# Optimization experiments

Measured on AMD Instinct MI355X. Metric: run time of the kernel, lower is better.

The kernel has to match this reference:

```python
import jax, jax.numpy as jnp
import numpy as np


def chamfer_bidirectional(p1, p2):
    """p1: [B,N,3], p2: [B,M,3]. Returns (min_sq_dist1 [B,N], min_sq_dist2 [B,M])."""
    # squared pairwise distances via ||a||^2 + ||b||^2 - 2 a.b  (avoids [B,N,M,3] diff tensor)
    n1 = jnp.sum(p1 * p1, axis=-1)          # [B,N]
    n2 = jnp.sum(p2 * p2, axis=-1)          # [B,M]
    cross = jnp.einsum('bnd,bmd->bnm', p1, p2)  # [B,N,M]
    d = n1[:, :, None] + n2[:, None, :] - 2.0 * cross  # [B,N,M]
    d = jnp.maximum(d, 0.0)
    return jnp.min(d, axis=2), jnp.min(d, axis=1)


def setup_inputs() -> dict:
    key = jax.random.key(0)
    k1, k2, k3, k4, k5 = jax.random.split(key, 5)
    B = 8
    return {
        'pred': jax.random.normal(k1, (B, 10, 3), dtype=jnp.float32),
        'target': jax.random.normal(k2, (B, 10, 3), dtype=jnp.float32),
        'coarse': jax.random.normal(k3, (B, 3, 1024), dtype=jnp.float32),
        'fine': jax.random.normal(k4, (B, 3, 4096), dtype=jnp.float32),
        'gt_pc': jax.random.normal(k5, (B, 4096, 3), dtype=jnp.float32),
    }


def reference(pred, target, coarse, fine, gt_pc):
    kp_loss = jnp.mean((pred - target) ** 2)
    c1, c2 = chamfer_bidirectional(jnp.transpose(coarse, (0, 2, 1)), gt_pc)
    f1, f2 = chamfer_bidirectional(jnp.transpose(fine, (0, 2, 1)), gt_pc)
    coarse_loss = jnp.mean(c1) + jnp.mean(c2)
    fine_loss = jnp.mean(f1) + jnp.mean(f2)
    return kp_loss + coarse_loss + fine_loss
```

## Files before the change

kernel.cpp:

```cpp
#include <hip/hip_runtime.h>
#include <math.h>

#define SBMAX 2112

template<int CHUNK, bool A_PLANAR, bool B_PLANAR>
__device__ __forceinline__ float chamfer_block(
    const float* __restrict__ A, int An,
    const float* __restrict__ B, int Bn,
    int lbid, float scale,
    float (&sb)[4][SBMAX], float (&red)[512])
{
    constexpr int NSEG    = 16;
    constexpr int SEG     = CHUNK / NSEG;
    constexpr int LOG_SEG = (CHUNK == 2048) ? 7 : 6;
    constexpr int SEGP    = SEG + 4;

    const int bpb   = An >> 5;
    const int batch = lbid / bpb;
    const int ablk  = lbid % bpb;
    const float* __restrict__ Ab = A + (size_t)batch * 3 * An;
    const float* __restrict__ Bb = B + (size_t)batch * 3 * Bn;

    const int tid  = threadIdx.x;
    const int slot = tid & 15;
    const int sp   = tid >> 4;
    const int p0   = ablk * 32 + slot;
    const int p1   = p0 + 16;

    float a0x, a0y, a0z, a1x, a1y, a1z;
    if (A_PLANAR) {
        a0x = Ab[p0];   a0y = Ab[An + p0];  a0z = Ab[2*An + p0];
        a1x = Ab[p1];   a1y = Ab[An + p1];  a1z = Ab[2*An + p1];
    } else {
        a0x = Ab[3*p0]; a0y = Ab[3*p0 + 1]; a0z = Ab[3*p0 + 2];
        a1x = Ab[3*p1]; a1y = Ab[3*p1 + 1]; a1z = Ab[3*p1 + 2];
    }
    const float a0s = fmaf(a0x, a0x, fmaf(a0y, a0y, a0z * a0z));
    const float a1s = fmaf(a1x, a1x, fmaf(a1y, a1y, a1z * a1z));

    const float BIG = 3.402823466e38f;
    float n00 = BIG, n01 = BIG, n10 = BIG, n11 = BIG;

    for (int t0 = 0; t0 < Bn; t0 += CHUNK) {
#pragma unroll
        for (int i = 0; i < CHUNK / 256; ++i) {
            const int k = tid + i * 256;
            float x, y, z;
            if (B_PLANAR) {
                x = Bb[t0 + k]; y = Bb[Bn + t0 + k]; z = Bb[2*Bn + t0 + k];
            } else {
                int base = 3 * (t0 + k);
                x = Bb[base]; y = Bb[base + 1]; z = Bb[base + 2];
            }
            const int addr = (k >> LOG_SEG) * SEGP + (k & (SEG - 1));
            sb[0][addr] = -2.0f * x;
            sb[1][addr] = -2.0f * y;
            sb[2][addr] = -2.0f * z;
            sb[3][addr] = fmaf(x, x, fmaf(y, y, z * z));
        }
        __syncthreads();

        const float4* __restrict__ px = (const float4*)&sb[0][sp * SEGP];
        const float4* __restrict__ py = (const float4*)&sb[1][sp * SEGP];
        const float4* __restrict__ pz = (const float4*)&sb[2][sp * SEGP];
        const float4* __restrict__ pw = (const float4*)&sb[3][sp * SEGP];
#pragma unroll 2
        for (int g = 0; g < SEG / 4; ++g) {
            float4 x = px[g], y = py[g], z = pz[g], w = pw[g];
            float d0, d1, d2, d3;
            d0 = fmaf(a0x, x.x, fmaf(a0y, y.x, fmaf(a0z, z.x, w.x)));
            d1 = fmaf(a0x, x.y, fmaf(a0y, y.y, fmaf(a0z, z.y, w.y)));
            d2 = fmaf(a0x, x.z, fmaf(a0y, y.z, fmaf(a0z, z.z, w.z)));
            d3 = fmaf(a0x, x.w, fmaf(a0y, y.w, fmaf(a0z, z.w, w.w)));
            n00 = fminf(fminf(d0, d1), n00);
            n01 = fminf(fminf(d2, d3), n01);
            d0 = fmaf(a1x, x.x, fmaf(a1y, y.x, fmaf(a1z, z.x, w.x)));
            d1 = fmaf(a1x, x.y, fmaf(a1y, y.y, fmaf(a1z, z.y, w.y)));
            d2 = fmaf(a1x, x.z, fmaf(a1y, y.z, fmaf(a1z, z.z, w.z)));
            d3 = fmaf(a1x, x.w, fmaf(a1y, y.w, fmaf(a1z, z.w, w.w)));
            n10 = fminf(fminf(d0, d1), n10);
            n11 = fminf(fminf(d2, d3), n11);
        }
        __syncthreads();
    }

    red[sp * 16 + slot]       = fminf(n00, n01);
    red[256 + sp * 16 + slot] = fminf(n10, n11);
    __syncthreads();
#pragma unroll
    for (int st = 8; st > 0; st >>= 1) {
        if (sp < st) {
            red[sp*16 + slot]       = fminf(red[sp*16 + slot],       red[(sp+st)*16 + slot]);
            red[256 + sp*16 + slot] = fminf(red[256 + sp*16 + slot], red[256 + (sp+st)*16 + slot]);
        }
        __syncthreads();
    }

    float contrib = 0.0f;
    if (tid < 16) {
        float d = fmaxf(0.0f, a0s + red[slot]) + fmaxf(0.0f, a1s + red[256 + slot]);
        d *= scale;
#pragma unroll
        for (int off = 8; off > 0; off >>= 1) d += __shfl_down(d, off, 16);
        contrib = d;
    }
    return contrib;
}

__device__ __forceinline__ float kp_block(const float* __restrict__ a,
                                          const float* __restrict__ b, int n,
                                          float (&red)[512])
{
    int tid = threadIdx.x;
    float s = 0.0f;
    for (int i = tid; i < n; i += 256) {
        float d = a[i] - b[i];
        s = fmaf(d, d, s);
    }
    for (int off = 32; off > 0; off >>= 1) s += __shfl_down(s, off, 64);
    if ((tid & 63) == 0) red[tid >> 6] = s;
    __syncthreads();
    float r = 0.0f;
    if (tid == 0) r = (red[0] + red[1] + red[2] + red[3]) / (float)n;
    return r;
}

__global__ __launch_bounds__(256, 4) void fused_all(
    const float* __restrict__ pred, const float* __restrict__ target, int nkp,
    const float* __restrict__ coarse, int Nc,
    const float* __restrict__ fine, int Nf,
    const float* __restrict__ gt, int M,
    int r1, int r2, int r3, int r4,
    float sc_f1, float sc_f2, float sc_c1, float sc_c2,
    float* __restrict__ ws)
{
    __shared__ __align__(16) float sb[4][SBMAX];
    __shared__ float red[512];
    const int bid = blockIdx.x;

    float contrib;
    if (bid < r1)
        contrib = chamfer_block<2048, true,  false>(fine,   Nf, gt,     M,  bid,      sc_f1, sb, red);
    else if (bid < r2)
        contrib = chamfer_block<2048, false, true >(gt,     M,  fine,   Nf, bid - r1, sc_f2, sb, red);
    else if (bid < r3)
        contrib = chamfer_block<2048, true,  false>(coarse, Nc, gt,     M,  bid - r2, sc_c1, sb, red);
    else if (bid < r4)
        contrib = chamfer_block<1024, false, true >(gt,     M,  coarse, Nc, bid - r3, sc_c2, sb, red);
    else
        contrib = kp_block(pred, target, nkp, red);

    if (threadIdx.x == 0) ws[bid] = contrib;
}

__global__ __launch_bounds__(256) void finalize(const float* __restrict__ ws, int n,
                                                float* __restrict__ out)
{
    int tid = threadIdx.x;
    float s = 0.0f;
    for (int i = tid; i < n; i += 256) s += ws[i];
    for (int off = 32; off > 0; off >>= 1) s += __shfl_down(s, off, 64);
    __shared__ float r[4];
    if ((tid & 63) == 0) r[tid >> 6] = s;
    __syncthreads();
    if (tid == 0) out[0] = r[0] + r[1] + r[2] + r[3];
}

extern "C" void kernel_launch(void* const* d_in, const int* in_sizes, int n_in,
                              void* d_out, int out_size, void* d_ws, size_t ws_size,
                              hipStream_t stream) {
    const float* pred   = (const float*)d_in[0];
    const float* target = (const float*)d_in[1];
    const float* coarse = (const float*)d_in[2];
    const float* fine   = (const float*)d_in[3];
    const float* gt     = (const float*)d_in[4];
    float* out = (float*)d_out;
    float* ws  = (float*)d_ws;

    const int nkp = in_sizes[0];
    const int B   = nkp / 30;
    const int Nc  = in_sizes[2] / (3 * B);
    const int Nf  = in_sizes[3] / (3 * B);
    const int M   = in_sizes[4] / (3 * B);

    const int r1 = B * (Nf / 32);
    const int r2 = r1 + B * (M / 32);
    const int r3 = r2 + B * (Nc / 32);
    const int r4 = r3 + B * (M / 32);
    const int nb = r4 + 1;

    fused_all<<<nb, 256, 0, stream>>>(
        pred, target, nkp, coarse, Nc, fine, Nf, gt, M,
        r1, r2, r3, r4,
        1.0f / (B * Nf), 1.0f / (B * M), 1.0f / (B * Nc), 1.0f / (B * M),
        ws);
    finalize<<<1, 256, 0, stream>>>(ws, nb, out);
}
```

Measured before the change: 97.66 us.

## Compute chamfer distances with bf16 MFMA using split hi/lo fragments

Adds a prebuild kernel that packs every point set into bf16 MFMA operand fragments. Each coordinate and squared norm is split into high and low bf16 parts so that one 16x16x32 bf16 MFMA yields the full squared distance at roughly float accuracy. A new MFMA kernel keeps running row minima in registers, reduces them across lanes, and merges them into global per-row minima with atomicMin. A final grid reduction with a completion counter produces the output. The path is used only for the exact test shapes; the old FP32 SIMD path stays as a fallback, and the bf16 split may lose precision.

```diff
diff --git a/kernel.cpp b/kernel.cpp
--- a/kernel.cpp
+++ b/kernel.cpp
@@ -1,104 +1,252 @@
 #include <hip/hip_runtime.h>
 #include <math.h>
 
+typedef __attribute__((ext_vector_type(8))) short bf16x8;
+typedef __attribute__((ext_vector_type(4))) float f32x4;
+typedef __attribute__((ext_vector_type(4))) unsigned int uint4v;
+
+#define ROWMIN_OFF 256
+#define N_ROWMIN   106496
+#define FRAG0      458752
+#define SZ_FINE    (8*256*1024)
+#define SZ_COARSE  (8*64*1024)
+#define OFF_FINEA  ((size_t)FRAG0)
+#define OFF_FINEB  ((size_t)FRAG0 + SZ_FINE)
+#define OFF_GTA    ((size_t)FRAG0 + 2*(size_t)SZ_FINE)
+#define OFF_GTB    ((size_t)FRAG0 + 3*(size_t)SZ_FINE)
+#define OFF_COARA  ((size_t)FRAG0 + 4*(size_t)SZ_FINE)
+#define OFF_COARB  ((size_t)FRAG0 + 4*(size_t)SZ_FINE + SZ_COARSE)
+#define WS_NEED    ((size_t)FRAG0 + 4*(size_t)SZ_FINE + 2*(size_t)SZ_COARSE)
+
+__device__ __forceinline__ unsigned short bf16_rn(float f) {
+    unsigned u = __float_as_uint(f);
+    u += 0x7FFFu + ((u >> 16) & 1u);
+    return (unsigned short)(u >> 16);
+}
+__device__ __forceinline__ float bf16_f(unsigned short h) {
+    return __uint_as_float(((unsigned)h) << 16);
+}
+
+__global__ __launch_bounds__(256) void prebuild(
+    const float* __restrict__ fine, const float* __restrict__ gt,
+    const float* __restrict__ coarse, unsigned* __restrict__ wsu)
+{
+    const int id = blockIdx.x * 256 + threadIdx.x;
+    const int FRAGU = 8 * 1152 * 64;
+    char* wsc = (char*)wsu;
+    if (id < FRAGU) {
+        const int lane = id & 63;
+        int t = (id >> 6) % 1152;
+        const int b = (id >> 6) / 1152;
+        const int role = (t >= 576) ? 1 : 0;
+        if (role) t -= 576;
+        float x, y, z; size_t outoff;
+        if (t < 256) {
+            const float* p = fine + (size_t)b * 3 * 4096;
+            int pt = t * 16 + (lane & 15);
+            x = p[pt]; y = p[4096 + pt]; z = p[8192 + pt];
+            outoff = (role ? OFF_FINEB : OFF_FINEA) + ((size_t)(b * 256 + t) * 64 + lane) * 16;
+        } else if (t < 512) {
+            int tile = t - 256;
+            const float* p = gt + (size_t)b * 4096 * 3;
+            int pt = tile * 16 + (lane & 15);
+            x = p[3 * pt]; y = p[3 * pt + 1]; z = p[3 * pt + 2];
+            outoff = (role ? OFF_GTB : OFF_GTA) + ((size_t)(b * 256 + tile) * 64 + lane) * 16;
+        } else {
+            int tile = t - 512;
+            const float* p = coarse + (size_t)b * 3 * 1024;
+            int pt = tile * 16 + (lane & 15);
+            x = p[pt]; y = p[1024 + pt]; z = p[2048 + pt];
+            outoff = (role ? OFF_COARB : OFF_COARA) + ((size_t)(b * 64 + tile) * 64 + lane) * 16;
+        }
+        const int kw = lane >> 4;
+        unsigned short hx = bf16_rn(x), hy = bf16_rn(y), hz = bf16_rn(z);
+        float fx = bf16_f(hx), fy = bf16_f(hy), fz = bf16_f(hz);
+        unsigned short lx = bf16_rn(x - fx), ly = bf16_rn(y - fy), lz = bf16_rn(z - fz);
+        float n = fmaf(x, x, fmaf(y, y, z * z));
+        unsigned short nh = bf16_rn(n);
+        unsigned short nl = bf16_rn(n - bf16_f(nh));
+        const unsigned short one = 0x3F80;
+        unsigned short e0=0,e1=0,e2=0,e3=0,e4=0,e5=0,e6=0,e7=0;
+        if (kw < 2) {
+            if (!role) {
+                unsigned short t0 = bf16_rn(-2.f * fx), t1 = bf16_rn(-2.f * fy), t2 = bf16_rn(-2.f * fz);
+                unsigned short u0 = bf16_rn(-2.f * bf16_f(lx)), u1 = bf16_rn(-2.f * bf16_f(ly)), u2 = bf16_rn(-2.f * bf16_f(lz));
+                if (kw == 0) { e0=t0; e1=t1; e2=t2; e3=t0; e4=t1; e5=t2; e6=u0; e7=u1; }
+                else         { e0=u2; e1=one; e2=one; e3=nh; e4=nl; }
+            } else {
+                if (kw == 0) { e0=hx; e1=hy; e2=hz; e3=lx; e4=ly; e5=lz; e6=hx; e7=hy; }
+                else         { e0=hz; e1=nh; e2=nl; e3=one; e4=one; }
+            }
+        }
+        uint4v v = { (unsigned)e0 | ((unsigned)e1 << 16),
+                     (unsigned)e2 | ((unsigned)e3 << 16),
+                     (unsigned)e4 | ((unsigned)e5 << 16),
+                     (unsigned)e6 | ((unsigned)e7 << 16) };
+        *(uint4v*)(wsc + outoff) = v;
+    } else if (id < FRAGU + N_ROWMIN) {
+        ((unsigned*)(wsc + ROWMIN_OFF))[id - FRAGU] = 0x7F800000u;
+    } else if (id == FRAGU + N_ROWMIN) {
+        wsu[0] = 0u;
+        wsu[1] = 0u;
+    }
+}
+
+__global__ __launch_bounds__(256, 4) void chamfer_mfma(unsigned char* __restrict__ wsb)
+{
+    const int w    = blockIdx.x * 4 + (threadIdx.x >> 6);
+    const int lane = threadIdx.x & 63;
+
+    int b, octet, ms, TA, TB, rowbase, rowsb;
+    size_t Aoff, Boff;
+    if (w < 2048)      { int u = w;        b = u >> 8; int r = u & 255; octet = r >> 3; ms = r & 7;
+                         Aoff = OFF_FINEA; TA = 256; Boff = OFF_GTB;   TB = 256; rowbase = 0;     rowsb = 4096; }
+    else if (w < 4096) { int u = w - 2048; b = u >> 8; int r = u & 255; octet = r >> 3; ms = r & 7;
+                         Aoff = OFF_GTA;   TA = 256; Boff = OFF_FINEB; TB = 256; rowbase = 32768; rowsb = 4096; }
+    else if (w < 4608) { int u = w - 4096; b = u >> 6; int r = u & 63;  octet = r >> 3; ms = r & 7;
+                         Aoff = OFF_COARA; TA = 64;  Boff = OFF_GTB;   TB = 256; rowbase = 65536; rowsb = 1024; }
+    else               { int u = w - 4608; b = u >> 6; int r = u & 63;  octet = r >> 1; ms = r & 1;
+                         Aoff = OFF_GTA;   TA = 256; Boff = OFF_COARB; TB = 64;  rowbase = 73728; rowsb = 4096; }
+
+    bf16x8 af[8];
+#pragma unroll
+    for (int s = 0; s < 8; ++s)
+        af[s] = *(const bf16x8*)(wsb + Aoff + ((size_t)((b * TA + octet * 8 + s) * 64 + lane)) * 16);
+
+    const unsigned char* bp = wsb + Boff + ((size_t)((b * TB + ms * 32) * 64 + lane)) * 16;
+
+    float rm[8][4];
+#pragma unroll
+    for (int s = 0; s < 8; ++s) { rm[s][0]=rm[s][1]=rm[s][2]=rm[s][3]=3.402823466e38f; }
+
+    const f32x4 zero = {0.f, 0.f, 0.f, 0.f};
+#pragma unroll 2
+    for (int mt = 0; mt < 32; ++mt) {
+        bf16x8 bf = *(const bf16x8*)(bp + (size_t)mt * 1024);
+#pragma unroll
+        for (int s = 0; s < 8; ++s) {
+            f32x4 r = __builtin_amdgcn_mfma_f32_16x16x32_bf16(af[s], bf, zero, 0, 0, 0);
+            rm[s][0] = fminf(rm[s][0], r[0]);
+            rm[s][1] = fminf(rm[s][1], r[1]);
+            rm[s][2] = fminf(rm[s][2], r[2]);
+            rm[s][3] = fminf(rm[s][3], r[3]);
+        }
+    }
+
+    unsigned* rowmin = (unsigned*)(wsb + ROWMIN_OFF);
+    const int rg = rowbase + b * rowsb + octet * 128;
+#pragma unroll
+    for (int s = 0; s < 8; ++s)
+#pragma unroll
+        for (int j = 0; j < 4; ++j) {
+            float v = fmaxf(rm[s][j], 0.f);
+            v = fminf(v, __shfl_xor(v, 1, 64));
+            v = fminf(v, __shfl_xor(v, 2, 64));
+            v = fminf(v, __shfl_xor(v, 4, 64));
+            v = fminf(v, __shfl_xor(v, 8, 64));
+            if ((lane & 15) == 0)
+                atomicMin(rowmin + rg + s * 16 + (lane >> 4) * 4 + j, __float_as_uint(v));
+        }
+}
+
+__global__ __launch_bounds__(256) void reduce_all(
+    unsigned* __restrict__ wsu,
+    const float* __restrict__ pred, const float* __restrict__ target,
+    float* __restrict__ out)
+{
+    const unsigned* rowmin = (const unsigned*)((const char*)wsu + ROWMIN_OFF);
+    const int tid = threadIdx.x;
+    float s = 0.f;
+    for (int i = blockIdx.x * 256 + tid; i < N_ROWMIN; i += gridDim.x * 256) {
+        float v = __uint_as_float(rowmin[i]);
+        float sc = (i >= 65536 && i < 73728) ? (1.f / 8192.f) : (1.f / 32768.f);
+        s = fmaf(v, sc, s);
+    }
+    if (blockIdx.x == 0 && tid < 240) {
+        float d = pred[tid] - target[tid];
+        s = fmaf(d, d * (1.f / 240.f), s);
+    }
+    for (int off = 32; off > 0; off >>= 1) s += __shfl_down(s, off, 64);
+    __shared__ float r4[4];
+    if ((tid & 63) == 0) r4[tid >> 6] = s;
+    __syncthreads();
+    if (tid == 0) {
+        atomicAdd((float*)wsu, r4[0] + r4[1] + r4[2] + r4[3]);
+        __threadfence();
+        unsigned old = atomicAdd(wsu + 1, 1u);
+        if (old == gridDim.x - 1) {
+            __threadfence();
+            out[0] = atomicAdd((float*)wsu, 0.f);
+        }
+    }
+}
+
 #define SBMAX 2112
-
 template<int CHUNK, bool A_PLANAR, bool B_PLANAR>
 __device__ __forceinline__ float chamfer_block(
-    const float* __restrict__ A, int An,
-    const float* __restrict__ B, int Bn,
-    int lbid, float scale,
-    float (&sb)[4][SBMAX], float (&red)[512])
-{
-    constexpr int NSEG    = 16;
-    constexpr int SEG     = CHUNK / NSEG;
+    const float* __restrict__ A, int An, const float* __restrict__ B, int Bn,
+    int lbid, float scale, float (&sb)[4][SBMAX], float (&red)[512])
+{
+    constexpr int NSEG = 16;
+    constexpr int SEG  = CHUNK / NSEG;
     constexpr int LOG_SEG = (CHUNK == 2048) ? 7 : 6;
-    constexpr int SEGP    = SEG + 4;
-
-    const int bpb   = An >> 5;
-    const int batch = lbid / bpb;
-    const int ablk  = lbid % bpb;
+    constexpr int SEGP = SEG + 4;
+    const int bpb = An >> 5, batch = lbid / bpb, ablk = lbid % bpb;
     const float* __restrict__ Ab = A + (size_t)batch * 3 * An;
     const float* __restrict__ Bb = B + (size_t)batch * 3 * Bn;
-
-    const int tid  = threadIdx.x;
-    const int slot = tid & 15;
-    const int sp   = tid >> 4;
-    const int p0   = ablk * 32 + slot;
-    const int p1   = p0 + 16;
-
+    const int tid = threadIdx.x, slot = tid & 15, sp = tid >> 4;
+    const int p0 = ablk * 32 + slot, p1 = p0 + 16;
     float a0x, a0y, a0z, a1x, a1y, a1z;
-    if (A_PLANAR) {
-        a0x = Ab[p0];   a0y = Ab[An + p0];  a0z = Ab[2*An + p0];
-        a1x = Ab[p1];   a1y = Ab[An + p1];  a1z = Ab[2*An + p1];
-    } else {
-        a0x = Ab[3*p0]; a0y = Ab[3*p0 + 1]; a0z = Ab[3*p0 + 2];
-        a1x = Ab[3*p1]; a1y = Ab[3*p1 + 1]; a1z = Ab[3*p1 + 2];
-    }
-    const float a0s = fmaf(a0x, a0x, fmaf(a0y, a0y, a0z * a0z));
-    const float a1s = fmaf(a1x, a1x, fmaf(a1y, a1y, a1z * a1z));
-
+    if (A_PLANAR) { a0x=Ab[p0]; a0y=Ab[An+p0]; a0z=Ab[2*An+p0]; a1x=Ab[p1]; a1y=Ab[An+p1]; a1z=Ab[2*An+p1]; }
+    else { a0x=Ab[3*p0]; a0y=Ab[3*p0+1]; a0z=Ab[3*p0+2]; a1x=Ab[3*p1]; a1y=Ab[3*p1+1]; a1z=Ab[3*p1+2]; }
+    const float a0s = fmaf(a0x,a0x,fmaf(a0y,a0y,a0z*a0z));
+    const float a1s = fmaf(a1x,a1x,fmaf(a1y,a1y,a1z*a1z));
     const float BIG = 3.402823466e38f;
-    float n00 = BIG, n01 = BIG, n10 = BIG, n11 = BIG;
-
+    float n00=BIG,n01=BIG,n10=BIG,n11=BIG;
     for (int t0 = 0; t0 < Bn; t0 += CHUNK) {
 #pragma unroll
         for (int i = 0; i < CHUNK / 256; ++i) {
-            const int k = tid + i * 256;
-            float x, y, z;
-            if (B_PLANAR) {
-                x = Bb[t0 + k]; y = Bb[Bn + t0 + k]; z = Bb[2*Bn + t0 + k];
-            } else {
-                int base = 3 * (t0 + k);
-                x = Bb[base]; y = Bb[base + 1]; z = Bb[base + 2];
-            }
+            const int k = tid + i * 256; float x, y, z;
+            if (B_PLANAR) { x=Bb[t0+k]; y=Bb[Bn+t0+k]; z=Bb[2*Bn+t0+k]; }
+            else { int base = 3*(t0+k); x=Bb[base]; y=Bb[base+1]; z=Bb[base+2]; }
             const int addr = (k >> LOG_SEG) * SEGP + (k & (SEG - 1));
-            sb[0][addr] = -2.0f * x;
-            sb[1][addr] = -2.0f * y;
-            sb[2][addr] = -2.0f * z;
-            sb[3][addr] = fmaf(x, x, fmaf(y, y, z * z));
+            sb[0][addr]=-2.f*x; sb[1][addr]=-2.f*y; sb[2][addr]=-2.f*z; sb[3][addr]=fmaf(x,x,fmaf(y,y,z*z));
         }
         __syncthreads();
-
-        const float4* __restrict__ px = (const float4*)&sb[0][sp * SEGP];
-        const float4* __restrict__ py = (const float4*)&sb[1][sp * SEGP];
-        const float4* __restrict__ pz = (const float4*)&sb[2][sp * SEGP];
-        const float4* __restrict__ pw = (const float4*)&sb[3][sp * SEGP];
+        const float4* px = (const float4*)&sb[0][sp*SEGP];
+        const float4* py = (const float4*)&sb[1][sp*SEGP];
+        const float4* pz = (const float4*)&sb[2][sp*SEGP];
+        const float4* pw = (const float4*)&sb[3][sp*SEGP];
 #pragma unroll 2
         for (int g = 0; g < SEG / 4; ++g) {
-            float4 x = px[g], y = py[g], z = pz[g], w = pw[g];
-            float d0, d1, d2, d3;
-            d0 = fmaf(a0x, x.x, fmaf(a0y, y.x, fmaf(a0z, z.x, w.x)));
-            d1 = fmaf(a0x, x.y, fmaf(a0y, y.y, fmaf(a0z, z.y, w.y)));
-            d2 = fmaf(a0x, x.z, fmaf(a0y, y.z, fmaf(a0z, z.z, w.z)));
-            d3 = fmaf(a0x, x.w, fmaf(a0y, y.w, fmaf(a0z, z.w, w.w)));
-            n00 = fminf(fminf(d0, d1), n00);
-            n01 = fminf(fminf(d2, d3), n01);
-            d0 = fmaf(a1x, x.x, fmaf(a1y, y.x, fmaf(a1z, z.x, w.x)));
-            d1 = fmaf(a1x, x.y, fmaf(a1y, y.y, fmaf(a1z, z.y, w.y)));
-            d2 = fmaf(a1x, x.z, fmaf(a1y, y.z, fmaf(a1z, z.z, w.z)));
-            d3 = fmaf(a1x, x.w, fmaf(a1y, y.w, fmaf(a1z, z.w, w.w)));
-            n10 = fminf(fminf(d0, d1), n10);
-            n11 = fminf(fminf(d2, d3), n11);
+            float4 x=px[g], y=py[g], z=pz[g], w=pw[g];
+            float d0,d1,d2,d3;
+            d0=fmaf(a0x,x.x,fmaf(a0y,y.x,fmaf(a0z,z.x,w.x)));
+            d1=fmaf(a0x,x.y,fmaf(a0y,y.y,fmaf(a0z,z.y,w.y)));
+            d2=fmaf(a0x,x.z,fmaf(a0y,y.z,fmaf(a0z,z.z,w.z)));
+            d3=fmaf(a0x,x.w,fmaf(a0y,y.w,fmaf(a0z,z.w,w.w)));
+            n00=fminf(fminf(d0,d1),n00); n01=fminf(fminf(d2,d3),n01);
+            d0=fmaf(a1x,x.x,fmaf(a1y,y.x,fmaf(a1z,z.x,w.x)));
+            d1=fmaf(a1x,x.y,fmaf(a1y,y.y,fmaf(a1z,z.y,w.y)));
+            d2=fmaf(a1x,x.z,fmaf(a1y,y.z,fmaf(a1z,z.z,w.z)));
+            d3=fmaf(a1x,x.w,fmaf(a1y,y.w,fmaf(a1z,z.w,w.w)));
+            n10=fminf(fminf(d0,d1),n10); n11=fminf(fminf(d2,d3),n11);
         }
         __syncthreads();
     }
-
-    red[sp * 16 + slot]       = fminf(n00, n01);
-    red[256 + sp * 16 + slot] = fminf(n10, n11);
+    red[sp*16+slot]=fminf(n00,n01); red[256+sp*16+slot]=fminf(n10,n11);
     __syncthreads();
 #pragma unroll
     for (int st = 8; st > 0; st >>= 1) {
         if (sp < st) {
-            red[sp*16 + slot]       = fminf(red[sp*16 + slot],       red[(sp+st)*16 + slot]);
-            red[256 + sp*16 + slot] = fminf(red[256 + sp*16 + slot], red[256 + (sp+st)*16 + slot]);
+            red[sp*16+slot]=fminf(red[sp*16+slot],red[(sp+st)*16+slot]);
+            red[256+sp*16+slot]=fminf(red[256+sp*16+slot],red[256+(sp+st)*16+slot]);
         }
         __syncthreads();
     }
-
-    float contrib = 0.0f;
+    float contrib = 0.f;
     if (tid < 16) {
-        float d = fmaxf(0.0f, a0s + red[slot]) + fmaxf(0.0f, a1s + red[256 + slot]);
+        float d = fmaxf(0.f,a0s+red[slot]) + fmaxf(0.f,a1s+red[256+slot]);
         d *= scale;
 #pragma unroll
         for (int off = 8; off > 0; off >>= 1) d += __shfl_down(d, off, 16);
@@ -108,56 +256,40 @@
 }
 
 __device__ __forceinline__ float kp_block(const float* __restrict__ a,
-                                          const float* __restrict__ b, int n,
-                                          float (&red)[512])
-{
-    int tid = threadIdx.x;
-    float s = 0.0f;
-    for (int i = tid; i < n; i += 256) {
-        float d = a[i] - b[i];
-        s = fmaf(d, d, s);
-    }
+                                          const float* __restrict__ b, int n, float (&red)[512])
+{
+    int tid = threadIdx.x; float s = 0.f;
+    for (int i = tid; i < n; i += 256) { float d = a[i]-b[i]; s = fmaf(d,d,s); }
     for (int off = 32; off > 0; off >>= 1) s += __shfl_down(s, off, 64);
     if ((tid & 63) == 0) red[tid >> 6] = s;
     __syncthreads();
-    float r = 0.0f;
-    if (tid == 0) r = (red[0] + red[1] + red[2] + red[3]) / (float)n;
+    float r = 0.f;
+    if (tid == 0) r = (red[0]+red[1]+red[2]+red[3]) / (float)n;
     return r;
 }
 
 __global__ __launch_bounds__(256, 4) void fused_all(
     const float* __restrict__ pred, const float* __restrict__ target, int nkp,
-    const float* __restrict__ coarse, int Nc,
-    const float* __restrict__ fine, int Nf,
-    const float* __restrict__ gt, int M,
-    int r1, int r2, int r3, int r4,
-    float sc_f1, float sc_f2, float sc_c1, float sc_c2,
-    float* __restrict__ ws)
+    const float* __restrict__ coarse, int Nc, const float* __restrict__ fine, int Nf,
+    const float* __restrict__ gt, int M, int r1, int r2, int r3, int r4,
+    float sc_f1, float sc_f2, float sc_c1, float sc_c2, float* __restrict__ ws)
 {
     __shared__ __align__(16) float sb[4][SBMAX];
     __shared__ float red[512];
     const int bid = blockIdx.x;
-
     float contrib;
-    if (bid < r1)
-        contrib = chamfer_block<2048, true,  false>(fine,   Nf, gt,     M,  bid,      sc_f1, sb, red);
-    else if (bid < r2)
-        contrib = chamfer_block<2048, false, true >(gt,     M,  fine,   Nf, bid - r1, sc_f2, sb, red);
-    else if (bid < r3)
-        contrib = chamfer_block<2048, true,  false>(coarse, Nc, gt,     M,  bid - r2, sc_c1, sb, red);
-    else if (bid < r4)
-        contrib = chamfer_block<1024, false, true >(gt,     M,  coarse, Nc, bid - r3, sc_c2, sb, red);
-    else
-        contrib = kp_block(pred, target, nkp, red);
-
+    if (bid < r1)      contrib = chamfer_block<2048,true, false>(fine,  Nf, gt,     M,  bid,      sc_f1, sb, red);
+    else if (bid < r2) contrib = chamfer_block<2048,false,true >(gt,    M,  fine,   Nf, bid - r1, sc_f2, sb, red);
+    else if (bid < r3) contrib = chamfer_block<2048,true, false>(coarse,Nc, gt,     M,  bid - r2, sc_c1, sb, red);
+    else if (bid < r4) contrib = chamfer_block<1024,false,true >(gt,    M,  coarse, Nc, bid - r3, sc_c2, sb, red);
+    else               contrib = kp_block(pred, target, nkp, red);
     if (threadIdx.x == 0) ws[bid] = contrib;
 }
 
 __global__ __launch_bounds__(256) void finalize(const float* __restrict__ ws, int n,
                                                 float* __restrict__ out)
 {
-    int tid = threadIdx.x;
-    float s = 0.0f;
+    int tid = threadIdx.x; float s = 0.f;
     for (int i = tid; i < n; i += 256) s += ws[i];
     for (int off = 32; off > 0; off >>= 1) s += __shfl_down(s, off, 64);
     __shared__ float r[4];
@@ -175,7 +307,6 @@
     const float* fine   = (const float*)d_in[3];
     const float* gt     = (const float*)d_in[4];
     float* out = (float*)d_out;
-    float* ws  = (float*)d_ws;
 
     const int nkp = in_sizes[0];
     const int B   = nkp / 30;
@@ -183,16 +314,26 @@
     const int Nf  = in_sizes[3] / (3 * B);
     const int M   = in_sizes[4] / (3 * B);
 
-    const int r1 = B * (Nf / 32);
-    const int r2 = r1 + B * (M / 32);
-    const int r3 = r2 + B * (Nc / 32);
-    const int r4 = r3 + B * (M / 32);
-    const int nb = r4 + 1;
-
-    fused_all<<<nb, 256, 0, stream>>>(
-        pred, target, nkp, coarse, Nc, fine, Nf, gt, M,
-        r1, r2, r3, r4,
-        1.0f / (B * Nf), 1.0f / (B * M), 1.0f / (B * Nc), 1.0f / (B * M),
-        ws);
-    finalize<<<1, 256, 0, stream>>>(ws, nb, out);
-}
+    const bool mfma_ok = (B == 8 && Nc == 1024 && Nf == 4096 && M == 4096 &&
+                          ws_size >= WS_NEED);
+    if (mfma_ok) {
+        unsigned* wsu = (unsigned*)d_ws;
+        const int FRAGU = 8 * 1152 * 64;
+        const int pre_total = FRAGU + N_ROWMIN + 1;
+        prebuild<<<(pre_total + 255) / 256, 256, 0, stream>>>(fine, gt, coarse, wsu);
+        chamfer_mfma<<<1280, 256, 0, stream>>>((unsigned char*)d_ws);
+        reduce_all<<<120, 256, 0, stream>>>(wsu, pred, target, out);
+    } else {
+        float* ws = (float*)d_ws;
+        const int r1 = B * (Nf / 32);
+        const int r2 = r1 + B * (M / 32);
+        const int r3 = r2 + B * (Nc / 32);
+        const int r4 = r3 + B * (M / 32);
+        const int nb = r4 + 1;
+        fused_all<<<nb, 256, 0, stream>>>(
+            pred, target, nkp, coarse, Nc, fine, Nf, gt, M,
+            r1, r2, r3, r4,
+            1.0f / (B * Nf), 1.0f / (B * M), 1.0f / (B * Nc), 1.0f / (B * M), ws);
+        finalize<<<1, 256, 0, stream>>>(ws, nb, out);
+    }
+}
```

Result: no change. 99.18 us (+1.6%).
